# Optimization experiments

Hardware: AMD Instinct MI355X
Metric: run time of the kernel (lower is better)

The kernel has to match this reference:

```python
import jax, jax.numpy as jnp
import numpy as np

B, T, C, H = 4, 4096, 1024, 16
D = C // H  # head dim 64


def setup_inputs() -> dict:
    key = jax.random.key(0)
    ks = jax.random.split(key, 10)
    s = 1.0 / np.sqrt(C)
    return {
        "x": jax.random.normal(ks[0], (B, T, C), jnp.float32),
        "y": jax.random.normal(ks[1], (B, T, C), jnp.float32),
        "Wq": jax.random.normal(ks[2], (C, C), jnp.float32) * s,
        "bq": jnp.zeros((C,), jnp.float32),
        "Wk": jax.random.normal(ks[3], (C, C), jnp.float32) * s,
        "bk": jnp.zeros((C,), jnp.float32),
        "Wv": jax.random.normal(ks[4], (C, C), jnp.float32) * s,
        "bv": jnp.zeros((C,), jnp.float32),
        "Wp": jax.random.normal(ks[5], (C, C), jnp.float32) * s,
        "bp": jnp.zeros((C,), jnp.float32),
    }


def _heads(t):
    # [B, T, C] -> [B, H, T, D]
    b, n, c = t.shape
    return t.reshape(b, n, H, D).transpose(0, 2, 1, 3)


def reference(x, y, Wq, bq, Wk, bk, Wv, bv, Wp, bp):
    q = jax.nn.softmax(_heads(x @ Wq.T + bq), axis=-1)  # [B,H,T1,D]
    k = jax.nn.softmax(_heads(y @ Wk.T + bk), axis=-1)  # [B,H,T2,D]
    v = _heads(y @ Wv.T + bv)                            # [B,H,T2,D]
    k_cumsum = jnp.sum(k, axis=-2, keepdims=True)        # [B,H,1,D]
    D_inv = 1.0 / jnp.sum(q * k_cumsum, axis=-1, keepdims=True)  # [B,H,T1,1]
    kv = jnp.einsum('bhnd,bhne->bhde', k, v)             # [B,H,D,D]
    out = q + jnp.einsum('bhnd,bhde->bhne', q, kv) * D_inv
    out = out.transpose(0, 2, 1, 3).reshape(x.shape[0], x.shape[1], C)
    return out @ Wp.T + bp
```

## Files before the change

kernel.cpp:

```cpp
#include <hip/hip_runtime.h>
#include <stdint.h>


typedef __attribute__((ext_vector_type(8))) short    bf16x8;
typedef __attribute__((ext_vector_type(4))) float    f32x4;
typedef __attribute__((ext_vector_type(8))) uint16_t u16x8;

typedef __attribute__((address_space(3))) uint32_t        as3_u32;
typedef const __attribute__((address_space(1))) uint32_t  as1_u32;

__device__ __forceinline__ uint16_t f2bf(float f) {
  union { float f; uint32_t u; } v; v.f = f;
  uint32_t r = v.u + 0x7FFFu + ((v.u >> 16) & 1u);
  return (uint16_t)(r >> 16);
}
__device__ __forceinline__ float bf2f(uint16_t u) {
  union { uint32_t u; float f; } v; v.u = ((uint32_t)u) << 16;
  return v.f;
}
__device__ __forceinline__ void gld16(void* lds, const void* g) {
  __builtin_amdgcn_global_load_lds((as1_u32*)g, (as3_u32*)lds, 16, 0, 0);
}

__global__ void zero_f32(float* __restrict__ p, int n4) {
  const int i = (blockIdx.x * 256 + threadIdx.x) * 4;
  if (i < n4 * 4) {
    f32x4 z = {0.f, 0.f, 0.f, 0.f};
    *(f32x4*)(p + i) = z;
  }
}

__global__ void cvt_bf16(const float* __restrict__ in, uint16_t* __restrict__ out, int n) {
  int i = (blockIdx.x * 256 + threadIdx.x) * 8;
  const int stride = gridDim.x * 256 * 8;
  for (; i < n; i += stride) {
    f32x4 a = *(const f32x4*)(in + i);
    f32x4 b = *(const f32x4*)(in + i + 4);
    u16x8 r;
    r[0] = f2bf(a[0]); r[1] = f2bf(a[1]); r[2] = f2bf(a[2]); r[3] = f2bf(a[3]);
    r[4] = f2bf(b[0]); r[5] = f2bf(b[1]); r[6] = f2bf(b[2]); r[7] = f2bf(b[3]);
    *(u16x8*)(out + i) = r;
  }
}

template<int MODE>
__global__ __launch_bounds__(256, 2)
void gemm_bt(const uint16_t* __restrict__ Ag, const uint16_t* __restrict__ Bg,
             uint16_t* __restrict__ outB, float* __restrict__ outF,
             const float* __restrict__ bias, float* __restrict__ kcum)
{
  __shared__ uint16_t Al[128 * 32];
  __shared__ uint16_t Bl[128 * 32];
  const int tid  = threadIdx.x;
  const int lane = tid & 63;
  const int w    = tid >> 6;
  const int wr   = w >> 1, wc = w & 1;
  const int lhi  = lane >> 4, llo = lane & 15;
  const int tM = blockIdx.x >> 3, tN = blockIdx.x & 7;
  const int rBase = tM << 7, cBase = tN << 7;

  f32x4 acc[4][4];
  const f32x4 z = {0.f, 0.f, 0.f, 0.f};
#pragma unroll
  for (int i = 0; i < 4; ++i)
#pragma unroll
    for (int j = 0; j < 4; ++j) acc[i][j] = z;

  const int linear = tid * 16;
  const int srow = linear >> 6;
  const int scol = linear & 63;
  const char* gA = (const char*)Ag + ((size_t)(rBase + srow) * 1024) * 2 + scol;
  const char* gB = (const char*)Bg + ((size_t)(cBase + srow) * 1024) * 2 + scol;
  char* lA = (char*)Al + linear;
  char* lB = (char*)Bl + linear;

  for (int kt = 0; kt < 1024; kt += 32) {
    if (kt) __syncthreads();
    gld16(lA,        gA + kt * 2);
    gld16(lA + 4096, gA + kt * 2 + (size_t)64 * 2048);
    gld16(lB,        gB + kt * 2);
    gld16(lB + 4096, gB + kt * 2 + (size_t)64 * 2048);
    __syncthreads();
    bf16x8 af[4], bfr[4];
#pragma unroll
    for (int mi = 0; mi < 4; ++mi)
      af[mi] = *(const bf16x8*)&Al[(wr * 64 + mi * 16 + llo) * 32 + lhi * 8];
#pragma unroll
    for (int ni = 0; ni < 4; ++ni)
      bfr[ni] = *(const bf16x8*)&Bl[(wc * 64 + ni * 16 + llo) * 32 + lhi * 8];
#pragma unroll
    for (int mi = 0; mi < 4; ++mi)
#pragma unroll
      for (int ni = 0; ni < 4; ++ni)
        acc[mi][ni] = __builtin_amdgcn_mfma_f32_16x16x32_bf16(af[mi], bfr[ni], acc[mi][ni], 0, 0, 0);
  }

  const int cW = cBase + wc * 64;
  const int rW = rBase + wr * 64;

  float bv[4];
#pragma unroll
  for (int ni = 0; ni < 4; ++ni) bv[ni] = bias[cW + ni * 16 + llo];
#pragma unroll
  for (int mi = 0; mi < 4; ++mi)
#pragma unroll
    for (int ni = 0; ni < 4; ++ni)
#pragma unroll
      for (int j = 0; j < 4; ++j) acc[mi][ni][j] += bv[ni];

  if (MODE == 1 || MODE == 2) {
#pragma unroll
    for (int mi = 0; mi < 4; ++mi)
#pragma unroll
      for (int j = 0; j < 4; ++j) {
        float mx = fmaxf(fmaxf(acc[mi][0][j], acc[mi][1][j]),
                         fmaxf(acc[mi][2][j], acc[mi][3][j]));
        mx = fmaxf(mx, __shfl_xor(mx, 1));
        mx = fmaxf(mx, __shfl_xor(mx, 2));
        mx = fmaxf(mx, __shfl_xor(mx, 4));
        mx = fmaxf(mx, __shfl_xor(mx, 8));
        float e0 = __expf(acc[mi][0][j] - mx);
        float e1 = __expf(acc[mi][1][j] - mx);
        float e2 = __expf(acc[mi][2][j] - mx);
        float e3 = __expf(acc[mi][3][j] - mx);
        float s = e0 + e1 + e2 + e3;
        s += __shfl_xor(s, 1);
        s += __shfl_xor(s, 2);
        s += __shfl_xor(s, 4);
        s += __shfl_xor(s, 8);
        float inv = 1.f / s;
        acc[mi][0][j] = e0 * inv; acc[mi][1][j] = e1 * inv;
        acc[mi][2][j] = e2 * inv; acc[mi][3][j] = e3 * inv;
      }
  }

  float cs[4] = {0.f, 0.f, 0.f, 0.f};
#pragma unroll
  for (int mi = 0; mi < 4; ++mi)
#pragma unroll
    for (int j = 0; j < 4; ++j) {
      const int rG = rW + mi * 16 + lhi * 4 + j;
#pragma unroll
      for (int ni = 0; ni < 4; ++ni) {
        const float v = acc[mi][ni][j];
        const int cG = cW + ni * 16 + llo;
        if (MODE == 3) outF[(size_t)rG * 1024 + cG] = v;
        else           outB[(size_t)rG * 1024 + cG] = f2bf(v);
        if (MODE == 2) cs[ni] += v;
      }
    }

  if (MODE == 2) {
    const int b = rBase >> 12;
#pragma unroll
    for (int ni = 0; ni < 4; ++ni) {
      float s = cs[ni];
      s += __shfl_xor(s, 16);
      s += __shfl_xor(s, 32);
      if (lhi == 0) atomicAdd(&kcum[b * 1024 + cW + ni * 16 + llo], s);
    }
  }
}

__global__ __launch_bounds__(256, 2)
void kv_outer(const uint16_t* __restrict__ kb, const uint16_t* __restrict__ vb,
              float* __restrict__ kvg)
{
  __shared__ uint16_t kT[4][64 * 32];
  __shared__ uint16_t vT[4][64 * 32];
  __shared__ float kvs[64 * 64];
  const int tid = threadIdx.x, lane = tid & 63, w = tid >> 6;
  const int lhi = lane >> 4, llo = lane & 15;
  const int head = blockIdx.x >> 3, chunk = blockIdx.x & 7;
  const int b = head >> 4, h = head & 15;

#pragma unroll
  for (int i = 0; i < 16; ++i) kvs[i * 256 + tid] = 0.f;
  __syncthreads();

  f32x4 acc[4][4];
  const f32x4 z = {0.f, 0.f, 0.f, 0.f};
#pragma unroll
  for (int i = 0; i < 4; ++i)
#pragma unroll
    for (int j = 0; j < 4; ++j) acc[i][j] = z;

  const size_t gbase = (size_t)b * 4096 * 1024 + (size_t)h * 64;
  for (int ks = 0; ks < 4; ++ks) {
    const int t0 = chunk * 512 + w * 128 + ks * 32;
#pragma unroll
    for (int p = 0; p < 4; ++p) {
      const int idx = (p * 64 + lane) * 8;
      const int t  = idx >> 6;
      const int d0 = idx & 63;
      u16x8 kr = *(const u16x8*)&kb[gbase + (size_t)(t0 + t) * 1024 + d0];
      u16x8 vr = *(const u16x8*)&vb[gbase + (size_t)(t0 + t) * 1024 + d0];
#pragma unroll
      for (int jj = 0; jj < 8; ++jj) {
        kT[w][(d0 + jj) * 32 + t] = kr[jj];
        vT[w][(d0 + jj) * 32 + t] = vr[jj];
      }
    }
    bf16x8 af[4], bfr[4];
#pragma unroll
    for (int mi = 0; mi < 4; ++mi)
      af[mi] = *(const bf16x8*)&kT[w][(mi * 16 + llo) * 32 + lhi * 8];
#pragma unroll
    for (int ni = 0; ni < 4; ++ni)
      bfr[ni] = *(const bf16x8*)&vT[w][(ni * 16 + llo) * 32 + lhi * 8];
#pragma unroll
    for (int mi = 0; mi < 4; ++mi)
#pragma unroll
      for (int ni = 0; ni < 4; ++ni)
        acc[mi][ni] = __builtin_amdgcn_mfma_f32_16x16x32_bf16(af[mi], bfr[ni], acc[mi][ni], 0, 0, 0);
  }

  __syncthreads();
  for (int ww = 0; ww < 4; ++ww) {
    if (w == ww) {
#pragma unroll
      for (int mi = 0; mi < 4; ++mi)
#pragma unroll
        for (int j = 0; j < 4; ++j) {
          const int d = mi * 16 + lhi * 4 + j;
#pragma unroll
          for (int ni = 0; ni < 4; ++ni)
            kvs[d * 64 + ni * 16 + llo] += acc[mi][ni][j];
        }
    }
    __syncthreads();
  }
  float* dst = kvg + (size_t)head * 4096;
#pragma unroll
  for (int i = 0; i < 16; ++i) atomicAdd(&dst[i * 256 + tid], kvs[i * 256 + tid]);
}

__global__ __launch_bounds__(256, 2)
void apply_attn(uint16_t* __restrict__ qb, const float* __restrict__ kvg,
                const float* __restrict__ kcum)
{
  __shared__ uint16_t ql[128 * 64];
  __shared__ uint16_t kvl[64 * 64];
  __shared__ float kcs[64];
  __shared__ float dinv[128];
  const int tid = threadIdx.x, lane = tid & 63, w = tid >> 6;
  const int lhi = lane >> 4, llo = lane & 15;
  const int head = blockIdx.x >> 5, tb = blockIdx.x & 31;
  const int b = head >> 4, h = head & 15;
  const int tBase = tb * 128;

  const char* qg = (const char*)qb + (((size_t)b * 4096 + tBase) * 1024 + h * 64) * 2;
#pragma unroll
  for (int p = 0; p < 4; ++p) {
    const int linear = (p * 256 + tid) * 16;
    const int r = linear >> 7, cb2 = linear & 127;
    gld16((char*)ql + linear, qg + (size_t)r * 2048 + cb2);
  }
  const float* kvh = kvg + (size_t)head * 4096;
#pragma unroll
  for (int i = 0; i < 16; ++i) {
    const int idx = i * 256 + tid;
    kvl[(idx & 63) * 64 + (idx >> 6)] = f2bf(kvh[idx]);
  }
  if (tid < 64) kcs[tid] = kcum[b * 1024 + h * 64 + tid];
  __syncthreads();

  {
    const int r = tid >> 1, half = tid & 1;
    float s = 0.f;
#pragma unroll
    for (int jj = 0; jj < 4; ++jj) {
      u16x8 q8 = *(const u16x8*)&ql[r * 64 + half * 32 + jj * 8];
#pragma unroll
      for (int m = 0; m < 8; ++m) s += bf2f(q8[m]) * kcs[half * 32 + jj * 8 + m];
    }
    s += __shfl_xor(s, 1);
    if (half == 0) dinv[r] = 1.f / s;
  }
  __syncthreads();

  f32x4 acc[2][4];
  const f32x4 z = {0.f, 0.f, 0.f, 0.f};
#pragma unroll
  for (int i = 0; i < 2; ++i)
#pragma unroll
    for (int j = 0; j < 4; ++j) acc[i][j] = z;

#pragma unroll
  for (int ks = 0; ks < 2; ++ks) {
    bf16x8 af[2], bfr[4];
#pragma unroll
    for (int mi = 0; mi < 2; ++mi)
      af[mi] = *(const bf16x8*)&ql[(w * 32 + mi * 16 + llo) * 64 + ks * 32 + lhi * 8];
#pragma unroll
    for (int ni = 0; ni < 4; ++ni)
      bfr[ni] = *(const bf16x8*)&kvl[(ni * 16 + llo) * 64 + ks * 32 + lhi * 8];
#pragma unroll
    for (int mi = 0; mi < 2; ++mi)
#pragma unroll
      for (int ni = 0; ni < 4; ++ni)
        acc[mi][ni] = __builtin_amdgcn_mfma_f32_16x16x32_bf16(af[mi], bfr[ni], acc[mi][ni], 0, 0, 0);
  }

#pragma unroll
  for (int mi = 0; mi < 2; ++mi)
#pragma unroll
    for (int j = 0; j < 4; ++j) {
      const int r = w * 32 + mi * 16 + lhi * 4 + j;
      const float di = dinv[r];
#pragma unroll
      for (int ni = 0; ni < 4; ++ni) {
        const int e = ni * 16 + llo;
        const float o = bf2f(ql[r * 64 + e]) + acc[mi][ni][j] * di;
        qb[((size_t)b * 4096 + tBase + r) * 1024 + h * 64 + e] = f2bf(o);
      }
    }
}

extern "C" void kernel_launch(void* const* d_in, const int* in_sizes, int n_in,
                              void* d_out, int out_size, void* d_ws, size_t ws_size,
                              hipStream_t stream) {
  const float* x  = (const float*)d_in[0];
  const float* y  = (const float*)d_in[1];
  const float* Wq = (const float*)d_in[2];
  const float* bq = (const float*)d_in[3];
  const float* Wk = (const float*)d_in[4];
  const float* bk = (const float*)d_in[5];
  const float* Wv = (const float*)d_in[6];
  const float* bv = (const float*)d_in[7];
  const float* Wp = (const float*)d_in[8];
  const float* bp = (const float*)d_in[9];
  float* out = (float*)d_out;
  char* ws   = (char*)d_ws;
  char* ob   = (char*)d_out;

  constexpr size_t MB = 1024 * 1024;
  constexpr int NELM = 16384 * 1024;

  uint16_t* xb  = (uint16_t*)(ob);
  uint16_t* yb  = (uint16_t*)(ob + 32 * MB);
  uint16_t* kb  = xb;
  uint16_t* vb  = (uint16_t*)(ws);
  uint16_t* qb  = (uint16_t*)(ws + 32 * MB);
  uint16_t* wqb = (uint16_t*)(ws + 64 * MB);
  uint16_t* wkb = (uint16_t*)(ws + 66 * MB);
  uint16_t* wvb = (uint16_t*)(ws + 68 * MB);
  uint16_t* wpb = (uint16_t*)(ws + 70 * MB);
  float*    kvf = (float*)   (ws + 72 * MB);
  float*    kcm = (float*)   (ws + 73 * MB);
  (void)ws_size; (void)in_sizes; (void)n_in; (void)out_size;

  zero_f32<<<260, 256, 0, stream>>>(kvf, 266240 / 4);

  cvt_bf16<<<2048, 256, 0, stream>>>(x,  xb,  NELM);
  cvt_bf16<<<2048, 256, 0, stream>>>(y,  yb,  NELM);
  cvt_bf16<<<512,  256, 0, stream>>>(Wq, wqb, 1024 * 1024);
  cvt_bf16<<<512,  256, 0, stream>>>(Wk, wkb, 1024 * 1024);
  cvt_bf16<<<512,  256, 0, stream>>>(Wv, wvb, 1024 * 1024);
  cvt_bf16<<<512,  256, 0, stream>>>(Wp, wpb, 1024 * 1024);

  gemm_bt<1><<<1024, 256, 0, stream>>>(xb, wqb, qb, nullptr, bq, nullptr);
  gemm_bt<2><<<1024, 256, 0, stream>>>(yb, wkb, kb, nullptr, bk, kcm);
  gemm_bt<0><<<1024, 256, 0, stream>>>(yb, wvb, vb, nullptr, bv, nullptr);

  kv_outer<<<512, 256, 0, stream>>>(kb, vb, kvf);
  apply_attn<<<2048, 256, 0, stream>>>(qb, kvf, kcm);

  gemm_bt<3><<<1024, 256, 0, stream>>>(qb, wpb, nullptr, out, bp, nullptr);
}
```

Measured before the change: 457.0 us.

## Fuse conversions, batch QKV GEMMs, and use pipelined 256x256 GEMM tiles

Merges the six fp32-to-bf16 conversions and the accumulator zeroing into one kernel. Replaces the 128x128 GEMM with a 512-thread 256x256-tile kernel that uses a 4-slot global_load_lds ring buffer with swizzled LDS layout, explicit waitcnt/barrier scheduling, and setprio around MFMA blocks. The Q, K and V projections now run as one launch indexed by block, with a swizzled tile order for L2 reuse. This cuts launch count and global reloads and overlaps loads with MFMA, at the cost of 128KB LDS per block, more registers, and only 256 blocks for the output projection.

```diff
diff --git a/kernel.cpp b/kernel.cpp
--- a/kernel.cpp
+++ b/kernel.cpp
@@ -22,95 +22,159 @@
   __builtin_amdgcn_global_load_lds((as1_u32*)g, (as3_u32*)lds, 16, 0, 0);
 }
 
-__global__ void zero_f32(float* __restrict__ p, int n4) {
-  const int i = (blockIdx.x * 256 + threadIdx.x) * 4;
-  if (i < n4 * 4) {
-    f32x4 z = {0.f, 0.f, 0.f, 0.f};
-    *(f32x4*)(p + i) = z;
-  }
-}
-
-__global__ void cvt_bf16(const float* __restrict__ in, uint16_t* __restrict__ out, int n) {
-  int i = (blockIdx.x * 256 + threadIdx.x) * 8;
-  const int stride = gridDim.x * 256 * 8;
-  for (; i < n; i += stride) {
-    f32x4 a = *(const f32x4*)(in + i);
-    f32x4 b = *(const f32x4*)(in + i + 4);
-    u16x8 r;
-    r[0] = f2bf(a[0]); r[1] = f2bf(a[1]); r[2] = f2bf(a[2]); r[3] = f2bf(a[3]);
-    r[4] = f2bf(b[0]); r[5] = f2bf(b[1]); r[6] = f2bf(b[2]); r[7] = f2bf(b[3]);
-    *(u16x8*)(out + i) = r;
-  }
-}
-
-template<int MODE>
-__global__ __launch_bounds__(256, 2)
-void gemm_bt(const uint16_t* __restrict__ Ag, const uint16_t* __restrict__ Bg,
-             uint16_t* __restrict__ outB, float* __restrict__ outF,
-             const float* __restrict__ bias, float* __restrict__ kcum)
-{
-  __shared__ uint16_t Al[128 * 32];
-  __shared__ uint16_t Bl[128 * 32];
-  const int tid  = threadIdx.x;
-  const int lane = tid & 63;
-  const int w    = tid >> 6;
-  const int wr   = w >> 1, wc = w & 1;
-  const int lhi  = lane >> 4, llo = lane & 15;
-  const int tM = blockIdx.x >> 3, tN = blockIdx.x & 7;
-  const int rBase = tM << 7, cBase = tN << 7;
-
-  f32x4 acc[4][4];
+struct CvtArgs {
+  const float* src[6];
+  uint16_t*    dst[6];
+  float*       zp;
+};
+__global__ void cvt_fused(CvtArgs a) {
+  const int total = 4751872;
+  int g = blockIdx.x * 256 + threadIdx.x;
+  for (; g < total; g += gridDim.x * 256) {
+    if (g < 4718592) {
+      int seg, off;
+      if (g < 4194304) { seg = g >> 21;            off = g & 2097151; }
+      else             { int t = g - 4194304; seg = 2 + (t >> 17); off = t & 131071; }
+      const float* s = a.src[seg] + (size_t)off * 8;
+      f32x4 lo = *(const f32x4*)s;
+      f32x4 hi = *(const f32x4*)(s + 4);
+      u16x8 r;
+      r[0]=f2bf(lo[0]); r[1]=f2bf(lo[1]); r[2]=f2bf(lo[2]); r[3]=f2bf(lo[3]);
+      r[4]=f2bf(hi[0]); r[5]=f2bf(hi[1]); r[6]=f2bf(hi[2]); r[7]=f2bf(hi[3]);
+      *(u16x8*)(a.dst[seg] + (size_t)off * 8) = r;
+    } else {
+      float* z = a.zp + (size_t)(g - 4718592) * 8;
+      f32x4 zz = {0.f, 0.f, 0.f, 0.f};
+      *(f32x4*)z = zz; *(f32x4*)(z + 4) = zz;
+    }
+  }
+}
+
+struct GemmPtrs {
+  const uint16_t* A;
+  const uint16_t* W;
+  uint16_t* outB;
+  float*    outF;
+  const float* bias;
+  float*    kcum;
+  int       mode;
+};
+struct GemmArgs { GemmPtrs p[3]; };
+
+__device__ __forceinline__ int lds_byte(int r, int g) {
+  return ((r >> 1) << 7) | (((g ^ ((r >> 1) & 3))) << 5) | ((r & 1) << 4);
+}
+
+#define NKT 32
+
+__global__ __launch_bounds__(512, 2)
+void gemm256(GemmArgs args) {
+  extern __shared__ char smem[];
+  const int idx = blockIdx.x >> 8;
+  const GemmPtrs gp = args.p[idx];
+  const int bin = blockIdx.x & 255;
+  const int swz = (bin & 7) * 32 + (bin >> 3);
+  const int tM = swz >> 2, tN = swz & 3;
+  const int rBase = tM << 8, cBase = tN << 8;
+
+  const int tid = threadIdx.x;
+  const int lane = tid & 63, w = tid >> 6;
+  const int wr = w >> 2, wc = w & 3;
+  const int lhi = lane >> 4, llo = lane & 15;
+
+  int pL[2]; size_t goA[2], goB[2];
+#pragma unroll
+  for (int j = 0; j < 2; ++j) {
+    const int p = (j * 512 + tid) * 16;
+    const int P = p >> 7, G = (p >> 5) & 3, h = (p >> 4) & 1;
+    const int r = P * 2 + h, g = G ^ (P & 3);
+    pL[j] = p;
+    goA[j] = ((size_t)(rBase + r) * 1024 + g * 8) * 2;
+    goB[j] = ((size_t)(cBase + r) * 1024 + g * 8) * 2;
+  }
+  const char* Ab = (const char*)gp.A;
+  const char* Wb = (const char*)gp.W;
+
+  int roA[8], roB[4];
+#pragma unroll
+  for (int mi = 0; mi < 8; ++mi) roA[mi] = lds_byte(wr * 128 + mi * 16 + llo, lhi);
+#pragma unroll
+  for (int ni = 0; ni < 4; ++ni) roB[ni] = 16384 + lds_byte(wc * 64 + ni * 16 + llo, lhi);
+
+  f32x4 acc[8][4];
   const f32x4 z = {0.f, 0.f, 0.f, 0.f};
 #pragma unroll
-  for (int i = 0; i < 4; ++i)
+  for (int i = 0; i < 8; ++i)
 #pragma unroll
     for (int j = 0; j < 4; ++j) acc[i][j] = z;
 
-  const int linear = tid * 16;
-  const int srow = linear >> 6;
-  const int scol = linear & 63;
-  const char* gA = (const char*)Ag + ((size_t)(rBase + srow) * 1024) * 2 + scol;
-  const char* gB = (const char*)Bg + ((size_t)(cBase + srow) * 1024) * 2 + scol;
-  char* lA = (char*)Al + linear;
-  char* lB = (char*)Bl + linear;
-
-  for (int kt = 0; kt < 1024; kt += 32) {
-    if (kt) __syncthreads();
-    gld16(lA,        gA + kt * 2);
-    gld16(lA + 4096, gA + kt * 2 + (size_t)64 * 2048);
-    gld16(lB,        gB + kt * 2);
-    gld16(lB + 4096, gB + kt * 2 + (size_t)64 * 2048);
-    __syncthreads();
-    bf16x8 af[4], bfr[4];
+#define STAGE_A(kt, slot) do { char* sb = smem + (slot) * 32768; \
+    gld16(sb + pL[0], Ab + goA[0] + (kt) * 64); \
+    gld16(sb + pL[1], Ab + goA[1] + (kt) * 64); } while (0)
+#define STAGE_B(kt, slot) do { char* sb = smem + (slot) * 32768 + 16384; \
+    gld16(sb + pL[0], Wb + goB[0] + (kt) * 64); \
+    gld16(sb + pL[1], Wb + goB[1] + (kt) * 64); } while (0)
+
+  STAGE_A(0, 0); STAGE_B(0, 0);
+  STAGE_A(1, 1); STAGE_B(1, 1);
+
+  bf16x8 a0[4], a1[4], bfr[4];
+  for (int kt = 0; kt < NKT; ++kt) {
+    if (kt < NKT - 1) asm volatile("s_waitcnt vmcnt(4)" ::: "memory");
+    else              asm volatile("s_waitcnt vmcnt(0)" ::: "memory");
+    __builtin_amdgcn_sched_barrier(0);
+    __builtin_amdgcn_s_barrier();
+    __builtin_amdgcn_sched_barrier(0);
+
+    const char* sA = smem + (kt & 3) * 32768;
+    const int pslot = (kt + 2) & 3;
+    const bool stg = (kt + 2) < NKT;
+
+#pragma unroll
+    for (int mi = 0; mi < 4; ++mi) a0[mi] = *(const bf16x8*)(sA + roA[mi]);
+#pragma unroll
+    for (int ni = 0; ni < 4; ++ni) bfr[ni] = *(const bf16x8*)(sA + roB[ni]);
+    if (stg) STAGE_A(kt + 2, pslot);
+    __builtin_amdgcn_s_setprio(1);
 #pragma unroll
     for (int mi = 0; mi < 4; ++mi)
-      af[mi] = *(const bf16x8*)&Al[(wr * 64 + mi * 16 + llo) * 32 + lhi * 8];
+#pragma unroll
+      for (int ni = 0; ni < 4; ++ni)
+        acc[mi][ni] = __builtin_amdgcn_mfma_f32_16x16x32_bf16(a0[mi], bfr[ni], acc[mi][ni], 0, 0, 0);
+    __builtin_amdgcn_s_setprio(0);
+    __builtin_amdgcn_sched_barrier(0);
+
+#pragma unroll
+    for (int mi = 0; mi < 4; ++mi) a1[mi] = *(const bf16x8*)(sA + roA[4 + mi]);
+    if (stg) STAGE_B(kt + 2, pslot);
+    __builtin_amdgcn_s_setprio(1);
+#pragma unroll
+    for (int mi = 0; mi < 4; ++mi)
+#pragma unroll
+      for (int ni = 0; ni < 4; ++ni)
+        acc[4 + mi][ni] = __builtin_amdgcn_mfma_f32_16x16x32_bf16(a1[mi], bfr[ni], acc[4 + mi][ni], 0, 0, 0);
+    __builtin_amdgcn_s_setprio(0);
+  }
+#undef STAGE_A
+#undef STAGE_B
+
+  const int mode = gp.mode;
+  const int cW = cBase + wc * 64;
+  const int rW = rBase + wr * 128;
+
+  float bv[4];
+#pragma unroll
+  for (int ni = 0; ni < 4; ++ni) bv[ni] = gp.bias[cW + ni * 16 + llo];
+#pragma unroll
+  for (int mi = 0; mi < 8; ++mi)
 #pragma unroll
     for (int ni = 0; ni < 4; ++ni)
-      bfr[ni] = *(const bf16x8*)&Bl[(wc * 64 + ni * 16 + llo) * 32 + lhi * 8];
-#pragma unroll
-    for (int mi = 0; mi < 4; ++mi)
-#pragma unroll
-      for (int ni = 0; ni < 4; ++ni)
-        acc[mi][ni] = __builtin_amdgcn_mfma_f32_16x16x32_bf16(af[mi], bfr[ni], acc[mi][ni], 0, 0, 0);
-  }
-
-  const int cW = cBase + wc * 64;
-  const int rW = rBase + wr * 64;
-
-  float bv[4];
-#pragma unroll
-  for (int ni = 0; ni < 4; ++ni) bv[ni] = bias[cW + ni * 16 + llo];
-#pragma unroll
-  for (int mi = 0; mi < 4; ++mi)
-#pragma unroll
-    for (int ni = 0; ni < 4; ++ni)
 #pragma unroll
       for (int j = 0; j < 4; ++j) acc[mi][ni][j] += bv[ni];
 
-  if (MODE == 1 || MODE == 2) {
-#pragma unroll
-    for (int mi = 0; mi < 4; ++mi)
+  if (mode == 1 || mode == 2) {
+#pragma unroll
+    for (int mi = 0; mi < 8; ++mi)
 #pragma unroll
       for (int j = 0; j < 4; ++j) {
         float mx = fmaxf(fmaxf(acc[mi][0][j], acc[mi][1][j]),
@@ -136,7 +200,7 @@
 
   float cs[4] = {0.f, 0.f, 0.f, 0.f};
 #pragma unroll
-  for (int mi = 0; mi < 4; ++mi)
+  for (int mi = 0; mi < 8; ++mi)
 #pragma unroll
     for (int j = 0; j < 4; ++j) {
       const int rG = rW + mi * 16 + lhi * 4 + j;
@@ -144,20 +208,20 @@
       for (int ni = 0; ni < 4; ++ni) {
         const float v = acc[mi][ni][j];
         const int cG = cW + ni * 16 + llo;
-        if (MODE == 3) outF[(size_t)rG * 1024 + cG] = v;
-        else           outB[(size_t)rG * 1024 + cG] = f2bf(v);
-        if (MODE == 2) cs[ni] += v;
+        if (mode == 3) gp.outF[(size_t)rG * 1024 + cG] = v;
+        else           gp.outB[(size_t)rG * 1024 + cG] = f2bf(v);
+        if (mode == 2) cs[ni] += v;
       }
     }
 
-  if (MODE == 2) {
+  if (mode == 2) {
     const int b = rBase >> 12;
 #pragma unroll
     for (int ni = 0; ni < 4; ++ni) {
       float s = cs[ni];
       s += __shfl_xor(s, 16);
       s += __shfl_xor(s, 32);
-      if (lhi == 0) atomicAdd(&kcum[b * 1024 + cW + ni * 16 + llo], s);
+      if (lhi == 0) atomicAdd(&gp.kcum[b * 1024 + cW + ni * 16 + llo], s);
     }
   }
 }
@@ -333,10 +397,9 @@
   float* out = (float*)d_out;
   char* ws   = (char*)d_ws;
   char* ob   = (char*)d_out;
+  (void)in_sizes; (void)n_in; (void)out_size; (void)ws_size;
 
   constexpr size_t MB = 1024 * 1024;
-  constexpr int NELM = 16384 * 1024;
-
   uint16_t* xb  = (uint16_t*)(ob);
   uint16_t* yb  = (uint16_t*)(ob + 32 * MB);
   uint16_t* kb  = xb;
@@ -348,23 +411,31 @@
   uint16_t* wpb = (uint16_t*)(ws + 70 * MB);
   float*    kvf = (float*)   (ws + 72 * MB);
   float*    kcm = (float*)   (ws + 73 * MB);
-  (void)ws_size; (void)in_sizes; (void)n_in; (void)out_size;
-
-  zero_f32<<<260, 256, 0, stream>>>(kvf, 266240 / 4);
-
-  cvt_bf16<<<2048, 256, 0, stream>>>(x,  xb,  NELM);
-  cvt_bf16<<<2048, 256, 0, stream>>>(y,  yb,  NELM);
-  cvt_bf16<<<512,  256, 0, stream>>>(Wq, wqb, 1024 * 1024);
-  cvt_bf16<<<512,  256, 0, stream>>>(Wk, wkb, 1024 * 1024);
-  cvt_bf16<<<512,  256, 0, stream>>>(Wv, wvb, 1024 * 1024);
-  cvt_bf16<<<512,  256, 0, stream>>>(Wp, wpb, 1024 * 1024);
-
-  gemm_bt<1><<<1024, 256, 0, stream>>>(xb, wqb, qb, nullptr, bq, nullptr);
-  gemm_bt<2><<<1024, 256, 0, stream>>>(yb, wkb, kb, nullptr, bk, kcm);
-  gemm_bt<0><<<1024, 256, 0, stream>>>(yb, wvb, vb, nullptr, bv, nullptr);
+
+  hipFuncSetAttribute((const void*)gemm256,
+                      hipFuncAttributeMaxDynamicSharedMemorySize, 131072);
+
+  CvtArgs ca;
+  ca.src[0] = x;  ca.dst[0] = xb;
+  ca.src[1] = y;  ca.dst[1] = yb;
+  ca.src[2] = Wq; ca.dst[2] = wqb;
+  ca.src[3] = Wk; ca.dst[3] = wkb;
+  ca.src[4] = Wv; ca.dst[4] = wvb;
+  ca.src[5] = Wp; ca.dst[5] = wpb;
+  ca.zp = kvf;
+  cvt_fused<<<2048, 256, 0, stream>>>(ca);
+
+  GemmArgs ga;
+  ga.p[0] = {xb, wqb, qb, nullptr, bq, nullptr, 1};
+  ga.p[1] = {yb, wkb, kb, nullptr, bk, kcm,     2};
+  ga.p[2] = {yb, wvb, vb, nullptr, bv, nullptr, 0};
+  gemm256<<<768, 512, 131072, stream>>>(ga);
 
   kv_outer<<<512, 256, 0, stream>>>(kb, vb, kvf);
   apply_attn<<<2048, 256, 0, stream>>>(qb, kvf, kcm);
 
-  gemm_bt<3><<<1024, 256, 0, stream>>>(qb, wpb, nullptr, out, bp, nullptr);
-}
+  GemmArgs gp2;
+  gp2.p[0] = {qb, wpb, nullptr, out, bp, nullptr, 3};
+  gp2.p[1] = gp2.p[0]; gp2.p[2] = gp2.p[0];
+  gemm256<<<256, 512, 131072, stream>>>(gp2);
+}
```

Measured after the change: 398.0 us. 12.9% less time.
